# Optimization experiments

Measured on AMD Instinct MI355X. Metric: run time of the kernel, lower is better.

Reference implementation:

```python
import jax, jax.numpy as jnp
import numpy as np

K_ORDER = 3
GRID_N = 10
GRID_LO, GRID_HI = -2.0, 2.0
LAYERS = [(49, 256), (256, 256), (256, 10)]
NCOEF = GRID_N + K_ORDER  # 13


def mish(x):
    return x * jnp.tanh(jax.nn.softplus(x))


def bspline_basis(x):
    # x: (B, in) -> basis (B, in, GRID_N + K_ORDER)
    h = (GRID_HI - GRID_LO) / GRID_N
    knots = GRID_LO + h * jnp.arange(-K_ORDER, GRID_N + K_ORDER + 1, dtype=x.dtype)  # (G+2k+1,)
    xx = x[..., None]
    B = ((xx >= knots[:-1]) & (xx < knots[1:])).astype(x.dtype)  # degree-0, (B,in,G+2k)
    for d in range(1, K_ORDER + 1):
        left = (xx - knots[: -(d + 1)]) / (knots[d:-1] - knots[: -(d + 1)]) * B[..., :-1]
        right = (knots[d + 1:] - xx) / (knots[d + 1:] - knots[1:-d]) * B[..., 1:]
        B = left + right
    return B  # (B, in, G+k)


def kan_layer(x, coef, scale_base, scale_sp, bias):
    # x: (B,in); coef: (in,out,G+k); scales: (in,out); bias: (out,)
    basis = bspline_basis(x)                                   # (B,in,G+k)
    spline = jnp.einsum('big,iog->bo', basis, coef * scale_sp[..., None])
    base = jnp.einsum('bi,io->bo', mish(x), scale_base)
    return base + spline + bias


def setup_inputs() -> dict:
    key = jax.random.key(0)
    ks = jax.random.split(key, 1 + 4 * len(LAYERS))
    inp = {'x': jax.random.normal(ks[0], (8192, 1, 28, 28), dtype=jnp.float32)}
    i = 1
    for li, (fin, fout) in enumerate(LAYERS, start=1):
        inp[f'coef{li}'] = 0.1 * jax.random.normal(ks[i], (fin, fout, NCOEF), dtype=jnp.float32); i += 1
        inp[f'sb{li}'] = 1.0 + 0.1 * jax.random.normal(ks[i], (fin, fout), dtype=jnp.float32); i += 1
        inp[f'sp{li}'] = 1.0 + 0.1 * jax.random.normal(ks[i], (fin, fout), dtype=jnp.float32); i += 1
        inp[f'b{li}'] = jnp.zeros((fout,), dtype=jnp.float32); i += 1
    return inp


def reference(x, coef1, sb1, sp1, b1, coef2, sb2, sp2, b2, coef3, sb3, sp3, b3):
    B = x.shape[0]
    # avg_pool2d(x, 4): 28x28 -> 7x7
    h = x.reshape(B, 1, 7, 4, 7, 4).mean(axis=(3, 5))
    h = h.reshape(B, 49)
    h = kan_layer(h, coef1, sb1, sp1, b1)
    h = kan_layer(h, coef2, sb2, sp2, b2)
    h = kan_layer(h, coef3, sb3, sp3, b3)
    return jax.nn.log_softmax(h, axis=1)
```

## Files before the change

kernel.cpp:

```cpp
#include <hip/hip_runtime.h>
#include <hip/hip_bf16.h>

typedef __bf16 bf16x8_t __attribute__((ext_vector_type(8)));
typedef float f32x4_t __attribute__((ext_vector_type(4)));
using bf16 = __hip_bfloat16;

__device__ __forceinline__ unsigned short f2bf_bits(float v) {
  __hip_bfloat16 h = __float2bfloat16(v);
  return *reinterpret_cast<unsigned short*>(&h);
}

__device__ __forceinline__ float mish_f(float x) {
  float z = __expf(x);
  float n = z * (z + 2.0f);
  float m = x * n / (n + 2.0f);
  return (x > 10.0f) ? x : m;
}

__device__ __forceinline__ void kan_feats28(bf16* dst, float x) {
  unsigned int* d32 = (unsigned int*)dst;
#pragma unroll
  for (int d = 0; d < 7; ++d) d32[d] = 0u;
  float t = (x + 3.2f) * 2.5f;
  if (t >= 0.0f && t < 16.0f) {
    float tf = floorf(t);
    int c = (int)tf;
    float u = t - tf;
    float um = 1.0f - u;
    float u2 = u * u, u3 = u2 * u;
    const float s6 = 1.0f / 6.0f;
    float w0 = um * um * um * s6;
    float w1 = (3.0f * u3 - 6.0f * u2 + 4.0f) * s6;
    float w2 = (-3.0f * u3 + 3.0f * u2 + 3.0f * u + 1.0f) * s6;
    float w3 = u3 * s6;
    int j0 = c - 3;
    if (j0 >= 0)               dst[j0]     = __float2bfloat16(w0);
    if (j0 >= -1 && j0 <= 11)  dst[j0 + 1] = __float2bfloat16(w1);
    if (j0 >= -2 && j0 <= 10)  dst[j0 + 2] = __float2bfloat16(w2);
    if (j0 <= 9)               dst[j0 + 3] = __float2bfloat16(w3);
  }
  dst[13] = __float2bfloat16(mish_f(x));
}

__global__ __launch_bounds__(256) void prep_all(
    const float* __restrict__ c1, const float* __restrict__ sb1, const float* __restrict__ sp1,
    const float* __restrict__ c2, const float* __restrict__ sb2, const float* __restrict__ sp2,
    const float* __restrict__ c3, const float* __restrict__ sb3, const float* __restrict__ sp3,
    bf16* __restrict__ W1f, bf16* __restrict__ W2f, bf16* __restrict__ W3f) {
  const int b = blockIdx.x, o = threadIdx.x;
  float vals[14];
  const int ntg = o >> 4, lrr = o & 15;
  if (b < 49) {
    const int i = b;
    const size_t io = (size_t)i * 256 + o;
    const float spv = sp1[io];
#pragma unroll
    for (int r = 0; r < 13; ++r) vals[r] = c1[io * 13 + r] * spv;
    vals[13] = sb1[io];
#pragma unroll
    for (int d = 0; d < 7; ++d) {
      const int k2 = i * 14 + 2 * d;
      const int s = k2 >> 5, r2 = k2 & 31;
      const size_t off = ((size_t)(s * 16 + ntg)) * 512 + lrr * 32 + (r2 >> 3) * 8 + (r2 & 7);
      *(unsigned int*)(W1f + off) = (unsigned int)f2bf_bits(vals[2 * d]) |
                                    ((unsigned int)f2bf_bits(vals[2 * d + 1]) << 16);
    }
  } else if (b == 49) {
#pragma unroll
    for (int d = 0; d < 9; ++d) {
      const int k2 = 686 + 2 * d;
      const int r2 = k2 & 31;
      *(unsigned int*)(W1f + ((size_t)(21 * 16 + ntg)) * 512 + lrr * 32 + (r2 >> 3) * 8 + (r2 & 7)) = 0u;
    }
  } else if (b < 306) {
    const int i = b - 50;
    const size_t io = (size_t)i * 256 + o;
    const float spv = sp2[io];
#pragma unroll
    for (int r = 0; r < 13; ++r) vals[r] = c2[io * 13 + r] * spv;
    vals[13] = sb2[io];
#pragma unroll
    for (int d = 0; d < 7; ++d) {
      const int k2 = i * 14 + 2 * d;
      const int s = k2 >> 5, r2 = k2 & 31;
      const size_t off = ((size_t)(s * 16 + ntg)) * 512 + lrr * 32 + (r2 >> 3) * 8 + (r2 & 7);
      *(unsigned int*)(W2f + off) = (unsigned int)f2bf_bits(vals[2 * d]) |
                                    ((unsigned int)f2bf_bits(vals[2 * d + 1]) << 16);
    }
  } else {
    const int i = b - 306;
    if (o < 10) {
      const size_t io = (size_t)i * 10 + o;
      const float spv = sp3[io];
#pragma unroll
      for (int r = 0; r < 13; ++r) vals[r] = c3[io * 13 + r] * spv;
      vals[13] = sb3[io];
#pragma unroll
      for (int d = 0; d < 7; ++d) {
        const int k2 = i * 14 + 2 * d;
        const int s = k2 >> 5, r2 = k2 & 31;
        const size_t off = (size_t)s * 512 + o * 32 + (r2 >> 3) * 8 + (r2 & 7);
        *(unsigned int*)(W3f + off) = (unsigned int)f2bf_bits(vals[2 * d]) |
                                      ((unsigned int)f2bf_bits(vals[2 * d + 1]) << 16);
      }
    } else if (o < 16) {
#pragma unroll
      for (int d = 0; d < 7; ++d) {
        const int k2 = i * 14 + 2 * d;
        const int s = k2 >> 5, r2 = k2 & 31;
        *(unsigned int*)(W3f + (size_t)s * 512 + o * 32 + (r2 >> 3) * 8 + (r2 & 7)) = 0u;
      }
    }
  }
}

__global__ __launch_bounds__(1024, 4) void meganet(
    const float* __restrict__ x, const bf16* __restrict__ W1f,
    const bf16* __restrict__ W2f, const bf16* __restrict__ W3f,
    const float* __restrict__ b1, const float* __restrict__ b2,
    const float* __restrict__ b3, float* __restrict__ out) {
  __shared__ __align__(16) char lds[73728];
  float* const Hs = (float*)lds;
  bf16* const Ach0 = (bf16*)(lds + 36864);
  bf16* const Ach1 = (bf16*)(lds + 51712);
  float* const P = (float*)(lds + 66560);
  float* const xs = (float*)lds;
  float* const Red = (float*)(lds + 36864);
  float* const V = (float*)(lds + 51712);

  const int t = threadIdx.x;
  const int w = t >> 6, lane = t & 63, quad = lane >> 4, lr = lane & 15;
  const int tr = t >> 4, ej = t & 15;
  const int r0 = blockIdx.x * 32;
  const int foff = lr * 32 + quad * 8;

  for (int h = 0; h < 2; ++h) {
    const float4* src = (const float4*)x + (size_t)(r0 + h * 16) * 196;
    float4* xd = (float4*)xs;
#pragma unroll
    for (int l = 0; l < 4; ++l) {
      const int idx = t + l * 1024;
      if (idx < 3136) xd[idx] = src[idx];
    }
    __syncthreads();
    if (t < 784) {
      const int img = t / 49, p = t - img * 49;
      const int oh = p / 7, ow = p - oh * 7;
      const float* xi = xs + img * 784 + oh * 112 + ow * 4;
      float s = 0.f;
#pragma unroll
      for (int rr = 0; rr < 4; ++rr)
#pragma unroll
        for (int cc = 0; cc < 4; ++cc) s += xi[rr * 28 + cc];
      P[(h * 16 + img) * 56 + p] = s * (1.0f / 16.0f);
    }
    __syncthreads();
  }

  f32x4_t acc1[2];
  acc1[0] = (f32x4_t){0.f, 0.f, 0.f, 0.f};
  acc1[1] = acc1[0];
  bf16x8_t q[4];
#pragma unroll
  for (int s = 0; s < 4; ++s)
    q[s] = *(const bf16x8_t*)(W1f + (size_t)(s * 16 + w) * 512 + foff);
  if (t < 512) kan_feats28(Ach0 + tr * 232 + ej * 14, P[tr * 56 + ej]);
  __syncthreads();
#pragma unroll
  for (int c = 0; c < 4; ++c) {
    const bf16* const Ac = (c & 1) ? Ach1 : Ach0;
    bf16* const An = (c & 1) ? Ach0 : Ach1;
    const int nks = (c < 3) ? 7 : 1;
#pragma unroll
    for (int ks = 0; ks < 7; ++ks) {
      if (ks >= nks) continue;
      const int kk = c * 7 + ks;
      const int sl = kk & 3;
      bf16x8_t bb = q[sl];
      if (kk + 4 < 22)
        q[sl] = *(const bf16x8_t*)(W1f + (size_t)((kk + 4) * 16 + w) * 512 + foff);
#pragma unroll
      for (int m = 0; m < 2; ++m) {
        bf16x8_t a = *(const bf16x8_t*)(Ac + (m * 16 + lr) * 232 + ks * 32 + quad * 8);
        acc1[m] = __builtin_amdgcn_mfma_f32_16x16x32_bf16(a, bb, acc1[m], 0, 0, 0);
      }
    }
    if (t < 512) {
      if (c < 2) {
        kan_feats28(An + tr * 232 + ej * 14, P[tr * 56 + (c + 1) * 16 + ej]);
      } else if (c == 2) {
        if (ej == 0) kan_feats28(An + tr * 232, P[tr * 56 + 48]);
        else if (ej == 1) {
          unsigned int* z = (unsigned int*)(An + tr * 232 + 14);
#pragma unroll
          for (int d = 0; d < 9; ++d) z[d] = 0u;
        }
      }
    }
    __syncthreads();
  }
  {
    const int col = w * 16 + lr;
    const float bn = b1[col];
#pragma unroll
    for (int m = 0; m < 2; ++m) {
      f32x4_t v;
#pragma unroll
      for (int r = 0; r < 4; ++r) v[r] = acc1[m][r] + bn;
      *(f32x4_t*)(Hs + col * 36 + m * 16 + quad * 4) = v;
    }
  }
  __syncthreads();

  f32x4_t acc2[2];
  acc2[0] = (f32x4_t){0.f, 0.f, 0.f, 0.f};
  acc2[1] = acc2[0];
#pragma unroll
  for (int s = 0; s < 4; ++s)
    q[s] = *(const bf16x8_t*)(W2f + (size_t)(s * 16 + w) * 512 + foff);
  if (t < 512) kan_feats28(Ach0 + tr * 232 + ej * 14, Hs[ej * 36 + tr]);
  __syncthreads();
#pragma unroll
  for (int c = 0; c < 16; ++c) {
    const bf16* const Ac = (c & 1) ? Ach1 : Ach0;
    bf16* const An = (c & 1) ? Ach0 : Ach1;
#pragma unroll
    for (int ks = 0; ks < 7; ++ks) {
      const int kk = c * 7 + ks;
      const int sl = kk & 3;
      bf16x8_t bb = q[sl];
      if (kk + 4 < 112)
        q[sl] = *(const bf16x8_t*)(W2f + (size_t)((kk + 4) * 16 + w) * 512 + foff);
#pragma unroll
      for (int m = 0; m < 2; ++m) {
        bf16x8_t a = *(const bf16x8_t*)(Ac + (m * 16 + lr) * 232 + ks * 32 + quad * 8);
        acc2[m] = __builtin_amdgcn_mfma_f32_16x16x32_bf16(a, bb, acc2[m], 0, 0, 0);
      }
    }
    if (t < 512 && c < 15)
      kan_feats28(An + tr * 232 + ej * 14, Hs[((c + 1) * 16 + ej) * 36 + tr]);
    __syncthreads();
  }
  {
    const int col = w * 16 + lr;
    const float bn = b2[col];
#pragma unroll
    for (int m = 0; m < 2; ++m) {
      f32x4_t v;
#pragma unroll
      for (int r = 0; r < 4; ++r) v[r] = acc2[m][r] + bn;
      *(f32x4_t*)(Hs + col * 36 + m * 16 + quad * 4) = v;
    }
  }
  __syncthreads();

  f32x4_t acc3 = {0.f, 0.f, 0.f, 0.f};
  const int mh = w / 7, ks3 = w % 7;
  bf16x8_t q3[2];
  if (w < 14) {
    q3[0] = *(const bf16x8_t*)(W3f + (size_t)ks3 * 512 + foff);
    q3[1] = *(const bf16x8_t*)(W3f + (size_t)(7 + ks3) * 512 + foff);
  }
  if (t < 512) kan_feats28(Ach0 + tr * 232 + ej * 14, Hs[ej * 36 + tr]);
  __syncthreads();
#pragma unroll
  for (int c = 0; c < 16; ++c) {
    const bf16* const Ac = (c & 1) ? Ach1 : Ach0;
    bf16* const An = (c & 1) ? Ach0 : Ach1;
    if (w < 14) {
      bf16x8_t bb = q3[c & 1];
      if (c + 2 < 16)
        q3[c & 1] = *(const bf16x8_t*)(W3f + (size_t)((c + 2) * 7 + ks3) * 512 + foff);
      bf16x8_t a = *(const bf16x8_t*)(Ac + (mh * 16 + lr) * 232 + ks3 * 32 + quad * 8);
      acc3 = __builtin_amdgcn_mfma_f32_16x16x32_bf16(a, bb, acc3, 0, 0, 0);
    }
    if (t < 512 && c < 15)
      kan_feats28(An + tr * 232 + ej * 14, Hs[((c + 1) * 16 + ej) * 36 + tr]);
    __syncthreads();
  }
  if (w < 14) {
#pragma unroll
    for (int r = 0; r < 4; ++r)
      Red[w * 256 + (quad * 4 + r) * 16 + lr] = acc3[r];
  }
  __syncthreads();
  if (t < 512 && tr < 32) {
    float s = (ej < 10) ? b3[ej] : 0.f;
    const int mh2 = tr >> 4, lrow = tr & 15;
#pragma unroll
    for (int ks = 0; ks < 7; ++ks) s += Red[(mh2 * 7 + ks) * 256 + lrow * 16 + ej];
    V[tr * 16 + ej] = s;
  }
  __syncthreads();
  if (t < 32) {
    float vv[10];
#pragma unroll
    for (int o = 0; o < 10; ++o) vv[o] = V[t * 16 + o];
    float mx = vv[0];
#pragma unroll
    for (int o = 1; o < 10; ++o) mx = fmaxf(mx, vv[o]);
    float se = 0.f;
#pragma unroll
    for (int o = 0; o < 10; ++o) se += expf(vv[o] - mx);
    const float l = mx + logf(se);
#pragma unroll
    for (int o = 0; o < 10; ++o) out[(size_t)(r0 + t) * 10 + o] = vv[o] - l;
  }
}

extern "C" void kernel_launch(void* const* d_in, const int* in_sizes, int n_in,
                              void* d_out, int out_size, void* d_ws, size_t ws_size,
                              hipStream_t stream) {
  const float* x = (const float*)d_in[0];
  const float* coef1 = (const float*)d_in[1];
  const float* sb1 = (const float*)d_in[2];
  const float* sp1 = (const float*)d_in[3];
  const float* b1 = (const float*)d_in[4];
  const float* coef2 = (const float*)d_in[5];
  const float* sb2 = (const float*)d_in[6];
  const float* sp2 = (const float*)d_in[7];
  const float* b2 = (const float*)d_in[8];
  const float* coef3 = (const float*)d_in[9];
  const float* sb3 = (const float*)d_in[10];
  const float* sp3 = (const float*)d_in[11];
  const float* b3 = (const float*)d_in[12];
  float* out = (float*)d_out;

  char* ws = (char*)d_ws;
  bf16* W1f = (bf16*)ws;
  bf16* W2f = (bf16*)(ws + 360448);
  bf16* W3f = (bf16*)(ws + 2195456);

  prep_all<<<562, 256, 0, stream>>>(coef1, sb1, sp1, coef2, sb2, sp2,
                                    coef3, sb3, sp3, W1f, W2f, W3f);
  meganet<<<256, 1024, 0, stream>>>(x, W1f, W2f, W3f, b1, b2, b3, out);
}
```

Measured before the change: 139.7 us.

## Split layer-2 K across warp groups and dedicate warps to basis generation

Layer 1 and layer 2 now tile the output as 2x2 MFMA blocks per warp. In layer 1 only the first eight warps compute, while the upper 512 threads generate the B-spline features, so feature generation no longer shares waves with MFMA work. In layer 2 the 7 K-steps per chunk are split 4/3 across the two warp groups, and the partial sums go to two separate LDS buffers that are added together when layer 3 builds its features. LDS use grows to about 124 KB per block, which limits occupancy, and layer 1 leaves half the warps idle during its MFMA phase.

Result: no change. 142.4 us (+2.0%).

```diff
diff --git a/kernel.cpp b/kernel.cpp
--- a/kernel.cpp
+++ b/kernel.cpp
@@ -119,20 +119,24 @@
     const bf16* __restrict__ W2f, const bf16* __restrict__ W3f,
     const float* __restrict__ b1, const float* __restrict__ b2,
     const float* __restrict__ b3, float* __restrict__ out) {
-  __shared__ __align__(16) char lds[73728];
-  float* const Hs = (float*)lds;
-  bf16* const Ach0 = (bf16*)(lds + 36864);
-  bf16* const Ach1 = (bf16*)(lds + 51712);
-  float* const P = (float*)(lds + 66560);
+  __shared__ __align__(16) char lds[126976];
+  float* const Hs0 = (float*)lds;
+  float* const Hs1 = (float*)(lds + 36864);
+  bf16* const Ach0 = (bf16*)(lds + 73728);
+  bf16* const Ach1 = (bf16*)(lds + 88576);
+  float* const P = (float*)(lds + 103424);
   float* const xs = (float*)lds;
-  float* const Red = (float*)(lds + 36864);
-  float* const V = (float*)(lds + 51712);
+  float* const Red = (float*)(lds + 110592);
+  float* const V = (float*)(lds + 124928);
 
   const int t = threadIdx.x;
   const int w = t >> 6, lane = t & 63, quad = lane >> 4, lr = lane & 15;
-  const int tr = t >> 4, ej = t & 15;
+  const int tr = (t >> 4) & 31, ej = t & 15;
   const int r0 = blockIdx.x * 32;
   const int foff = lr * 32 + quad * 8;
+  const int kg = w >> 3, ng = w & 7;
+  const int ntg0 = 2 * ng;
+  const int nks = kg ? 3 : 4, ks0 = kg ? 4 : 0;
 
   for (int h = 0; h < 2; ++h) {
     const float4* src = (const float4*)x + (size_t)(r0 + h * 16) * 196;
@@ -157,35 +161,47 @@
     __syncthreads();
   }
 
-  f32x4_t acc1[2];
-  acc1[0] = (f32x4_t){0.f, 0.f, 0.f, 0.f};
-  acc1[1] = acc1[0];
-  bf16x8_t q[4];
-#pragma unroll
-  for (int s = 0; s < 4; ++s)
-    q[s] = *(const bf16x8_t*)(W1f + (size_t)(s * 16 + w) * 512 + foff);
-  if (t < 512) kan_feats28(Ach0 + tr * 232 + ej * 14, P[tr * 56 + ej]);
+  f32x4_t acc[2][2];
+#pragma unroll
+  for (int m = 0; m < 2; ++m)
+#pragma unroll
+    for (int n = 0; n < 2; ++n) acc[m][n] = (f32x4_t){0.f, 0.f, 0.f, 0.f};
+
+  bf16x8_t q0[4], q1[4];
+  if (kg == 0) {
+#pragma unroll
+    for (int s = 0; s < 4; ++s) {
+      q0[s] = *(const bf16x8_t*)(W1f + (size_t)(s * 16 + ntg0) * 512 + foff);
+      q1[s] = *(const bf16x8_t*)(W1f + (size_t)(s * 16 + ntg0 + 1) * 512 + foff);
+    }
+  }
+  if (t >= 512) kan_feats28(Ach0 + tr * 232 + ej * 14, P[tr * 56 + ej]);
   __syncthreads();
 #pragma unroll
   for (int c = 0; c < 4; ++c) {
     const bf16* const Ac = (c & 1) ? Ach1 : Ach0;
     bf16* const An = (c & 1) ? Ach0 : Ach1;
-    const int nks = (c < 3) ? 7 : 1;
-#pragma unroll
-    for (int ks = 0; ks < 7; ++ks) {
-      if (ks >= nks) continue;
-      const int kk = c * 7 + ks;
-      const int sl = kk & 3;
-      bf16x8_t bb = q[sl];
-      if (kk + 4 < 22)
-        q[sl] = *(const bf16x8_t*)(W1f + (size_t)((kk + 4) * 16 + w) * 512 + foff);
-#pragma unroll
-      for (int m = 0; m < 2; ++m) {
-        bf16x8_t a = *(const bf16x8_t*)(Ac + (m * 16 + lr) * 232 + ks * 32 + quad * 8);
-        acc1[m] = __builtin_amdgcn_mfma_f32_16x16x32_bf16(a, bb, acc1[m], 0, 0, 0);
-      }
-    }
-    if (t < 512) {
+    const int nksc = (c < 3) ? 7 : 1;
+    if (kg == 0) {
+#pragma unroll
+      for (int ks = 0; ks < 7; ++ks) {
+        if (ks >= nksc) continue;
+        const int kk = c * 7 + ks;
+        const int sl = kk & 3;
+        bf16x8_t bb0 = q0[sl], bb1 = q1[sl];
+        if (kk + 4 < 22) {
+          q0[sl] = *(const bf16x8_t*)(W1f + (size_t)((kk + 4) * 16 + ntg0) * 512 + foff);
+          q1[sl] = *(const bf16x8_t*)(W1f + (size_t)((kk + 4) * 16 + ntg0 + 1) * 512 + foff);
+        }
+#pragma unroll
+        for (int m = 0; m < 2; ++m) {
+          bf16x8_t a = *(const bf16x8_t*)(Ac + (m * 16 + lr) * 232 + ks * 32 + quad * 8);
+          acc[m][0] = __builtin_amdgcn_mfma_f32_16x16x32_bf16(a, bb0, acc[m][0], 0, 0, 0);
+          acc[m][1] = __builtin_amdgcn_mfma_f32_16x16x32_bf16(a, bb1, acc[m][1], 0, 0, 0);
+        }
+      }
+    }
+    if (t >= 512) {
       if (c < 2) {
         kan_feats28(An + tr * 232 + ej * 14, P[tr * 56 + (c + 1) * 16 + ej]);
       } else if (c == 2) {
@@ -199,58 +215,73 @@
     }
     __syncthreads();
   }
-  {
-    const int col = w * 16 + lr;
-    const float bn = b1[col];
-#pragma unroll
-    for (int m = 0; m < 2; ++m) {
-      f32x4_t v;
-#pragma unroll
-      for (int r = 0; r < 4; ++r) v[r] = acc1[m][r] + bn;
-      *(f32x4_t*)(Hs + col * 36 + m * 16 + quad * 4) = v;
-    }
-  }
-  __syncthreads();
-
-  f32x4_t acc2[2];
-  acc2[0] = (f32x4_t){0.f, 0.f, 0.f, 0.f};
-  acc2[1] = acc2[0];
-#pragma unroll
-  for (int s = 0; s < 4; ++s)
-    q[s] = *(const bf16x8_t*)(W2f + (size_t)(s * 16 + w) * 512 + foff);
-  if (t < 512) kan_feats28(Ach0 + tr * 232 + ej * 14, Hs[ej * 36 + tr]);
+  if (kg == 0) {
+#pragma unroll
+    for (int m = 0; m < 2; ++m)
+#pragma unroll
+      for (int n = 0; n < 2; ++n) {
+        const int col = ng * 32 + n * 16 + lr;
+        const float bn = b1[col];
+        f32x4_t v;
+#pragma unroll
+        for (int r = 0; r < 4; ++r) v[r] = acc[m][n][r] + bn;
+        *(f32x4_t*)(Hs0 + col * 36 + m * 16 + quad * 4) = v;
+      }
+  }
+  __syncthreads();
+
+#pragma unroll
+  for (int m = 0; m < 2; ++m)
+#pragma unroll
+    for (int n = 0; n < 2; ++n) acc[m][n] = (f32x4_t){0.f, 0.f, 0.f, 0.f};
+  bf16x8_t c0[4], c1[4];
+#pragma unroll
+  for (int j = 0; j < 4; ++j) {
+    if (j < nks) {
+      const int kk = ks0 + j;
+      c0[j] = *(const bf16x8_t*)(W2f + (size_t)(kk * 16 + ntg0) * 512 + foff);
+      c1[j] = *(const bf16x8_t*)(W2f + (size_t)(kk * 16 + ntg0 + 1) * 512 + foff);
+    }
+  }
+  if (t >= 512) kan_feats28(Ach0 + tr * 232 + ej * 14, Hs0[ej * 36 + tr]);
   __syncthreads();
 #pragma unroll
   for (int c = 0; c < 16; ++c) {
     const bf16* const Ac = (c & 1) ? Ach1 : Ach0;
     bf16* const An = (c & 1) ? Ach0 : Ach1;
 #pragma unroll
-    for (int ks = 0; ks < 7; ++ks) {
-      const int kk = c * 7 + ks;
-      const int sl = kk & 3;
-      bf16x8_t bb = q[sl];
-      if (kk + 4 < 112)
-        q[sl] = *(const bf16x8_t*)(W2f + (size_t)((kk + 4) * 16 + w) * 512 + foff);
+    for (int j = 0; j < 4; ++j) {
+      if (j >= nks) continue;
+      const int kk = c * 7 + ks0 + j;
+      bf16x8_t bb0 = c0[j], bb1 = c1[j];
+      if (c < 15) {
+        c0[j] = *(const bf16x8_t*)(W2f + (size_t)((kk + 7) * 16 + ntg0) * 512 + foff);
+        c1[j] = *(const bf16x8_t*)(W2f + (size_t)((kk + 7) * 16 + ntg0 + 1) * 512 + foff);
+      }
 #pragma unroll
       for (int m = 0; m < 2; ++m) {
-        bf16x8_t a = *(const bf16x8_t*)(Ac + (m * 16 + lr) * 232 + ks * 32 + quad * 8);
-        acc2[m] = __builtin_amdgcn_mfma_f32_16x16x32_bf16(a, bb, acc2[m], 0, 0, 0);
-      }
-    }
-    if (t < 512 && c < 15)
-      kan_feats28(An + tr * 232 + ej * 14, Hs[((c + 1) * 16 + ej) * 36 + tr]);
+        bf16x8_t a = *(const bf16x8_t*)(Ac + (m * 16 + lr) * 232 + (ks0 + j) * 32 + quad * 8);
+        acc[m][0] = __builtin_amdgcn_mfma_f32_16x16x32_bf16(a, bb0, acc[m][0], 0, 0, 0);
+        acc[m][1] = __builtin_amdgcn_mfma_f32_16x16x32_bf16(a, bb1, acc[m][1], 0, 0, 0);
+      }
+    }
+    if (t >= 512 && c < 15)
+      kan_feats28(An + tr * 232 + ej * 14, Hs0[((c + 1) * 16 + ej) * 36 + tr]);
     __syncthreads();
   }
   {
-    const int col = w * 16 + lr;
-    const float bn = b2[col];
-#pragma unroll
-    for (int m = 0; m < 2; ++m) {
-      f32x4_t v;
-#pragma unroll
-      for (int r = 0; r < 4; ++r) v[r] = acc2[m][r] + bn;
-      *(f32x4_t*)(Hs + col * 36 + m * 16 + quad * 4) = v;
-    }
+    float* const Hd = kg ? Hs1 : Hs0;
+#pragma unroll
+    for (int m = 0; m < 2; ++m)
+#pragma unroll
+      for (int n = 0; n < 2; ++n) {
+        const int col = ng * 32 + n * 16 + lr;
+        const float bn = kg ? 0.f : b2[col];
+        f32x4_t v;
+#pragma unroll
+        for (int r = 0; r < 4; ++r) v[r] = acc[m][n][r] + bn;
+        *(f32x4_t*)(Hd + col * 36 + m * 16 + quad * 4) = v;
+      }
   }
   __syncthreads();
 
@@ -261,7 +292,7 @@
     q3[0] = *(const bf16x8_t*)(W3f + (size_t)ks3 * 512 + foff);
     q3[1] = *(const bf16x8_t*)(W3f + (size_t)(7 + ks3) * 512 + foff);
   }
-  if (t < 512) kan_feats28(Ach0 + tr * 232 + ej * 14, Hs[ej * 36 + tr]);
+  if (t < 512) kan_feats28(Ach0 + tr * 232 + ej * 14, Hs0[ej * 36 + tr] + Hs1[ej * 36 + tr]);
   __syncthreads();
 #pragma unroll
   for (int c = 0; c < 16; ++c) {
@@ -274,8 +305,10 @@
       bf16x8_t a = *(const bf16x8_t*)(Ac + (mh * 16 + lr) * 232 + ks3 * 32 + quad * 8);
       acc3 = __builtin_amdgcn_mfma_f32_16x16x32_bf16(a, bb, acc3, 0, 0, 0);
     }
-    if (t < 512 && c < 15)
-      kan_feats28(An + tr * 232 + ej * 14, Hs[((c + 1) * 16 + ej) * 36 + tr]);
+    if (t < 512 && c < 15) {
+      const int idx = ((c + 1) * 16 + ej) * 36 + tr;
+      kan_feats28(An + tr * 232 + ej * 14, Hs0[idx] + Hs1[idx]);
+    }
     __syncthreads();
   }
   if (w < 14) {
@@ -284,7 +317,7 @@
       Red[w * 256 + (quad * 4 + r) * 16 + lr] = acc3[r];
   }
   __syncthreads();
-  if (t < 512 && tr < 32) {
+  if (t < 512) {
     float s = (ej < 10) ? b3[ej] : 0.f;
     const int mh2 = tr >> 4, lrow = tr & 15;
 #pragma unroll
```

## Deepen weight prefetch ring and alternate feature-building warps across chunks

Applied to the files above, without the earlier changes.

Raises the register prefetch depth for the layer 1/2 weight fragments from 4 to 12 slots and for layer 3 from 2 to 4, so global weight loads have more time to arrive before their MFMAs. Feature generation for the next A chunk now alternates between the lower and upper half of the block each iteration, which spreads the VALU/LDS work across all waves instead of always the same eight. The layer-2 prep blocks are split in half with 128 active threads each, giving more, smaller prep blocks. The extra prefetch registers raise VGPR pressure under the 1024x4 launch bound and may cause spilling.

New measurement: 141.7 us. About the same (+1.4%).

```diff
diff --git a/kernel.cpp b/kernel.cpp
--- a/kernel.cpp
+++ b/kernel.cpp
@@ -47,11 +47,11 @@
     const float* __restrict__ c2, const float* __restrict__ sb2, const float* __restrict__ sp2,
     const float* __restrict__ c3, const float* __restrict__ sb3, const float* __restrict__ sp3,
     bf16* __restrict__ W1f, bf16* __restrict__ W2f, bf16* __restrict__ W3f) {
-  const int b = blockIdx.x, o = threadIdx.x;
+  const int b = blockIdx.x, t = threadIdx.x;
   float vals[14];
-  const int ntg = o >> 4, lrr = o & 15;
   if (b < 49) {
-    const int i = b;
+    const int i = b, o = t;
+    const int ntg = o >> 4, lrr = o & 15;
     const size_t io = (size_t)i * 256 + o;
     const float spv = sp1[io];
 #pragma unroll
@@ -66,14 +66,19 @@
                                     ((unsigned int)f2bf_bits(vals[2 * d + 1]) << 16);
     }
   } else if (b == 49) {
+    const int ntg = t >> 4, lrr = t & 15;
 #pragma unroll
     for (int d = 0; d < 9; ++d) {
       const int k2 = 686 + 2 * d;
       const int r2 = k2 & 31;
       *(unsigned int*)(W1f + ((size_t)(21 * 16 + ntg)) * 512 + lrr * 32 + (r2 >> 3) * 8 + (r2 & 7)) = 0u;
     }
-  } else if (b < 306) {
-    const int i = b - 50;
+  } else if (b < 562) {
+    if (t >= 128) return;
+    const int idx = b - 50;
+    const int i = idx >> 1;
+    const int o = (idx & 1) * 128 + t;
+    const int ntg = o >> 4, lrr = o & 15;
     const size_t io = (size_t)i * 256 + o;
     const float spv = sp2[io];
 #pragma unroll
@@ -88,7 +93,7 @@
                                     ((unsigned int)f2bf_bits(vals[2 * d + 1]) << 16);
     }
   } else {
-    const int i = b - 306;
+    const int i = b - 562, o = t;
     if (o < 10) {
       const size_t io = (size_t)i * 10 + o;
       const float spv = sp3[io];
@@ -130,7 +135,7 @@
 
   const int t = threadIdx.x;
   const int w = t >> 6, lane = t & 63, quad = lane >> 4, lr = lane & 15;
-  const int tr = t >> 4, ej = t & 15;
+  const int tr = t >> 5 >= 16 ? (t >> 4) & 31 : (t >> 4) & 31, ej = t & 15;
   const int r0 = blockIdx.x * 32;
   const int foff = lr * 32 + quad * 8;
 
@@ -160,11 +165,11 @@
   f32x4_t acc1[2];
   acc1[0] = (f32x4_t){0.f, 0.f, 0.f, 0.f};
   acc1[1] = acc1[0];
-  bf16x8_t q[4];
-#pragma unroll
-  for (int s = 0; s < 4; ++s)
+  bf16x8_t q[12];
+#pragma unroll
+  for (int s = 0; s < 12; ++s)
     q[s] = *(const bf16x8_t*)(W1f + (size_t)(s * 16 + w) * 512 + foff);
-  if (t < 512) kan_feats28(Ach0 + tr * 232 + ej * 14, P[tr * 56 + ej]);
+  if (t >= 512) kan_feats28(Ach0 + tr * 232 + ej * 14, P[tr * 56 + ej]);
   __syncthreads();
 #pragma unroll
   for (int c = 0; c < 4; ++c) {
@@ -175,17 +180,18 @@
     for (int ks = 0; ks < 7; ++ks) {
       if (ks >= nks) continue;
       const int kk = c * 7 + ks;
-      const int sl = kk & 3;
+      const int sl = kk % 12;
       bf16x8_t bb = q[sl];
-      if (kk + 4 < 22)
-        q[sl] = *(const bf16x8_t*)(W1f + (size_t)((kk + 4) * 16 + w) * 512 + foff);
+      if (kk + 12 < 22)
+        q[sl] = *(const bf16x8_t*)(W1f + (size_t)((kk + 12) * 16 + w) * 512 + foff);
 #pragma unroll
       for (int m = 0; m < 2; ++m) {
         bf16x8_t a = *(const bf16x8_t*)(Ac + (m * 16 + lr) * 232 + ks * 32 + quad * 8);
         acc1[m] = __builtin_amdgcn_mfma_f32_16x16x32_bf16(a, bb, acc1[m], 0, 0, 0);
       }
     }
-    if (t < 512) {
+    const bool doF = ((c & 1) == 0) ? (t < 512) : (t >= 512);
+    if (doF) {
       if (c < 2) {
         kan_feats28(An + tr * 232 + ej * 14, P[tr * 56 + (c + 1) * 16 + ej]);
       } else if (c == 2) {
@@ -216,9 +222,9 @@
   acc2[0] = (f32x4_t){0.f, 0.f, 0.f, 0.f};
   acc2[1] = acc2[0];
 #pragma unroll
-  for (int s = 0; s < 4; ++s)
+  for (int s = 0; s < 12; ++s)
     q[s] = *(const bf16x8_t*)(W2f + (size_t)(s * 16 + w) * 512 + foff);
-  if (t < 512) kan_feats28(Ach0 + tr * 232 + ej * 14, Hs[ej * 36 + tr]);
+  if (t >= 512) kan_feats28(Ach0 + tr * 232 + ej * 14, Hs[ej * 36 + tr]);
   __syncthreads();
 #pragma unroll
   for (int c = 0; c < 16; ++c) {
@@ -227,17 +233,18 @@
 #pragma unroll
     for (int ks = 0; ks < 7; ++ks) {
       const int kk = c * 7 + ks;
-      const int sl = kk & 3;
+      const int sl = kk % 12;
       bf16x8_t bb = q[sl];
-      if (kk + 4 < 112)
-        q[sl] = *(const bf16x8_t*)(W2f + (size_t)((kk + 4) * 16 + w) * 512 + foff);
+      if (kk + 12 < 112)
+        q[sl] = *(const bf16x8_t*)(W2f + (size_t)((kk + 12) * 16 + w) * 512 + foff);
 #pragma unroll
       for (int m = 0; m < 2; ++m) {
         bf16x8_t a = *(const bf16x8_t*)(Ac + (m * 16 + lr) * 232 + ks * 32 + quad * 8);
         acc2[m] = __builtin_amdgcn_mfma_f32_16x16x32_bf16(a, bb, acc2[m], 0, 0, 0);
       }
     }
-    if (t < 512 && c < 15)
+    const bool doF = ((c & 1) == 0) ? (t < 512) : (t >= 512);
+    if (doF && c < 15)
       kan_feats28(An + tr * 232 + ej * 14, Hs[((c + 1) * 16 + ej) * 36 + tr]);
     __syncthreads();
   }
@@ -256,10 +263,11 @@
 
   f32x4_t acc3 = {0.f, 0.f, 0.f, 0.f};
   const int mh = w / 7, ks3 = w % 7;
-  bf16x8_t q3[2];
+  bf16x8_t q3[4];
   if (w < 14) {
-    q3[0] = *(const bf16x8_t*)(W3f + (size_t)ks3 * 512 + foff);
-    q3[1] = *(const bf16x8_t*)(W3f + (size_t)(7 + ks3) * 512 + foff);
+#pragma unroll
+    for (int s = 0; s < 4; ++s)
+      q3[s] = *(const bf16x8_t*)(W3f + (size_t)(s * 7 + ks3) * 512 + foff);
   }
   if (t < 512) kan_feats28(Ach0 + tr * 232 + ej * 14, Hs[ej * 36 + tr]);
   __syncthreads();
@@ -268,13 +276,14 @@
     const bf16* const Ac = (c & 1) ? Ach1 : Ach0;
     bf16* const An = (c & 1) ? Ach0 : Ach1;
     if (w < 14) {
-      bf16x8_t bb = q3[c & 1];
-      if (c + 2 < 16)
-        q3[c & 1] = *(const bf16x8_t*)(W3f + (size_t)((c + 2) * 7 + ks3) * 512 + foff);
+      bf16x8_t bb = q3[c & 3];
+      if (c + 4 < 16)
+        q3[c & 3] = *(const bf16x8_t*)(W3f + (size_t)((c + 4) * 7 + ks3) * 512 + foff);
       bf16x8_t a = *(const bf16x8_t*)(Ac + (mh * 16 + lr) * 232 + ks3 * 32 + quad * 8);
       acc3 = __builtin_amdgcn_mfma_f32_16x16x32_bf16(a, bb, acc3, 0, 0, 0);
     }
-    if (t < 512 && c < 15)
+    const bool doF = ((c & 1) == 0) ? (t >= 512) : (t < 512);
+    if (doF && c < 15)
       kan_feats28(An + tr * 232 + ej * 14, Hs[((c + 1) * 16 + ej) * 36 + tr]);
     __syncthreads();
   }
@@ -284,7 +293,7 @@
       Red[w * 256 + (quad * 4 + r) * 16 + lr] = acc3[r];
   }
   __syncthreads();
-  if (t < 512 && tr < 32) {
+  if (t < 512) {
     float s = (ej < 10) ? b3[ej] : 0.f;
     const int mh2 = tr >> 4, lrow = tr & 15;
 #pragma unroll
@@ -331,7 +340,7 @@
   bf16* W2f = (bf16*)(ws + 360448);
   bf16* W3f = (bf16*)(ws + 2195456);
 
-  prep_all<<<562, 256, 0, stream>>>(coef1, sb1, sp1, coef2, sb2, sp2,
+  prep_all<<<818, 256, 0, stream>>>(coef1, sb1, sp1, coef2, sb2, sp2,
                                     coef3, sb3, sp3, W1f, W2f, W3f);
   meganet<<<256, 1024, 0, stream>>>(x, W1f, W2f, W3f, b1, b2, b3, out);
 }
```
